# Kernel tuning notes

Measured on AMD Instinct MI355X. Metric: run time of the kernel, lower is better.

## Reference

```python
import jax, jax.numpy as jnp
import numpy as np

# ---- constants mirroring the torch module ----
OSAMP = 8            # temporal oversampling factor
MAX_ITER = 10        # forward solver iterations (LBFGS replaced by fixed GD)
NEG_SHIFT = 2 * OSAMP
OTP = 5              # baseline frames subtracted from ctc/aif
C_SHARP = 500.0      # sharpness constant C=500 in fermi_ir_func
LR = 0.1             # fixed step size for the deterministic forward solve


def interp_linear_1d(x, size):
    # interp_linear_1D: linear upsampling along last (time) axis
    return jax.image.resize(x, x.shape[:-1] + (size,), method='linear')


def fermi_ir(eta, t_os):
    # eta: [B,3,H,W] = (amplitude A, decay rate k, delay t0); t_os: [Tos]
    tsh = t_os - t_os[NEG_SHIFT]                    # negative time shift
    A = eta[:, 0][..., None]                        # [B,H,W,1]
    k = eta[:, 1][..., None]
    t0 = eta[:, 2][..., None]
    step = jax.nn.sigmoid(C_SHARP * tsh)            # sharp causal onset (C=500)
    return A * jax.nn.sigmoid(k * (t0 - tsh)) * step  # [B,H,W,Tos]


def convolve(aif, ir):
    # linear convolution along time via FFT; output aligned with neg_shift offset
    Tos = ir.shape[-1]
    n = 2 * Tos
    Fa = jnp.fft.rfft(aif, n=n, axis=-1)            # [B,1,1,n/2+1]
    Fi = jnp.fft.rfft(ir, n=n, axis=-1)             # [B,H,W,n/2+1]
    full = jnp.fft.irfft(Fa * Fi, n=n, axis=-1)
    return jax.lax.dynamic_slice_in_dim(full, NEG_SHIFT, Tos, axis=-1)


def make_objective(ctc, aif, time, eta_prior, lambda_reg):
    # preprocessing from FermiDataConsLBFGS.forward
    aif = aif - aif[..., :OTP].mean(-1, keepdims=True)
    ctc = ctc - ctc[..., :OTP].mean(-1, keepdims=True)
    Tos = OSAMP * ctc.shape[-1]
    aif_os = interp_linear_1d(aif, Tos)
    ctc_os = interp_linear_1d(ctc, Tos)
    t_os = interp_linear_1d(time, Tos)
    ctc_dc = ctc_os[..., ::OSAMP]                   # [B,H,W,T]
    C_nn = (eta_prior ** 2).sum(axis=(0, 2, 3), keepdims=True)  # [1,3,1,1]
    C_dc = (ctc_dc ** 2).sum()
    sp_lam = jax.nn.softplus(lambda_reg).squeeze()

    def F_obj(eta):  # FermiDConsObj.__call__ (OD disabled: indx_dc = all frames)
        ir = fermi_ir(eta, t_os)
        ctc_est = convolve(aif_os, ir)[..., ::OSAMP] / OSAMP
        dc = ((ctc_dc - ctc_est) ** 2 / C_dc).sum()
        reg = sp_lam * (((eta - eta_prior) ** 2) / C_nn).sum()
        pos = (jax.nn.relu(-eta) ** 2).sum()
        return dc + reg + pos
    return F_obj


def setup_inputs():
    key = jax.random.key(0)
    k1, k2, k3, k4 = jax.random.split(key, 4)
    B, H, W, T = 1, 128, 128, 64
    ctc = jax.random.normal(k1, (B, H, W, T), jnp.float32) * 0.1
    aif = jax.random.uniform(k2, (B, 1, 1, T), jnp.float32)
    time = jnp.arange(T, dtype=jnp.float32)
    seg = jnp.ones((B, H, W), jnp.int32)
    eta_nn = jax.random.uniform(k3, (B, 3, H, W), jnp.float32)
    lambda_reg = jax.random.normal(k4, (1,), jnp.float32)
    return {"ctc": ctc, "aif": aif, "time": time, "seg": seg,
            "eta_nn": eta_nn, "lambda_reg": lambda_reg}


def reference(ctc, aif, time, seg, eta_nn, lambda_reg):
    # seg only affects the (disabled) outlier-detection path
    F_obj = make_objective(ctc, aif, time, eta_nn, lambda_reg)
    gradF = jax.grad(F_obj)

    def step(eta, _):
        return eta - LR * gradF(eta), None

    eta_pi, _ = jax.lax.scan(step, eta_nn, None, length=MAX_ITER)
    return eta_pi
```

## Files before the change

### kernel.cpp

```cpp
#include <hip/hip_runtime.h>
#include <math.h>

#define T_IN 64
#define NPIX 16384
#define MAX_ITER 10
#define NSLOT 43
#define MAGIC 0x13579BDFu

typedef _Float16 half8_t __attribute__((ext_vector_type(8)));
typedef __fp16   fp16x2  __attribute__((ext_vector_type(2)));
typedef float    f32x4   __attribute__((ext_vector_type(4)));
typedef int      i32x4   __attribute__((ext_vector_type(4)));

union H8 { half8_t v; fp16x2 h2[4]; i32x4 i4; };

__device__ __forceinline__ float rcp_fast(float x) { return __builtin_amdgcn_rcpf(x); }

__constant__ constexpr int NTMIN[16] = {0,0,0,0,0,1,1,1,1,2,2,2,2,3,3,3};
__constant__ constexpr int TOFS[16]  = {0,4,8,12,16,20,23,26,29,32,34,36,38,40,41,42};

template<int KT>
__device__ __forceinline__ void buildTile(float T0, float nK, float r, int q,
        const float (&d10b)[16], const float (&tse0)[8], const float (&tse15)[8],
        H8& F0h, H8& F1h, H8& F2h) {
    float  x[8];
    fp16x2 d1h[4];
    float  d10 = T0 - d10b[KT];
    const fp16x2 c1 = {(__fp16)0.25f, (__fp16)0.25f};
    const fp16x2 c2 = {(__fp16)0.50f, (__fp16)0.50f};
    const fp16x2 c3 = {(__fp16)0.75f, (__fp16)0.75f};
    bool arith = true;
    if constexpr (KT == 0 || KT == 15) {
        bool flat = (KT == 0) ? (q == 0) : (q == 3);
        if (flat) {
            arith = false;
            const float* te;
            if constexpr (KT == 0) te = tse0; else te = tse15;
            #pragma unroll
            for (int j = 0; j < 8; ++j) x[j] = __expf(nK * (T0 - te[j]));
            #pragma unroll
            for (int jj = 0; jj < 4; ++jj)
                d1h[jj] = __builtin_amdgcn_cvt_pkrtz(T0 - te[2*jj],
                                                     T0 - te[2*jj+1]);
        }
    }
    if (arith) {
        x[0] = __expf(nK * d10);
        x[4] = __expf(nK * (d10 - 0.5f));
        x[1] = x[0]*r; x[2] = x[1]*r; x[3] = x[2]*r;
        x[5] = x[4]*r; x[6] = x[5]*r; x[7] = x[6]*r;
        fp16x2 D0 = __builtin_amdgcn_cvt_pkrtz(d10, d10 - 0.125f);
        d1h[0] = D0;
        d1h[1] = D0 - c1;
        d1h[2] = D0 - c2;
        d1h[3] = D0 - c3;
    }
    #pragma unroll
    for (int jj = 0; jj < 4; ++jj) {
        float s1a = rcp_fast(1.0f + x[2*jj]);
        float s1b = rcp_fast(1.0f + x[2*jj+1]);
        fp16x2 sh = __builtin_amdgcn_cvt_pkrtz(s1a, s1b);
        fp16x2 eh = sh - sh*sh;
        F0h.h2[jj] = sh;
        F1h.h2[jj] = eh * d1h[jj];
        F2h.h2[jj] = eh;
    }
}

template<int KT>
struct Pipe2 {
    static __device__ __forceinline__ void run(float T0, float nK, float r, int q, int lane,
            const float (&d10b)[16], const float (&tse0)[8], const float (&tse15)[8],
            const i32x4* __restrict__ Bs,
            H8 (&F0p)[2], H8 (&F1p)[2], H8 (&F2p)[2],
            f32x4 (&acc)[3][4]) {
        constexpr int PB = (KT >> 1) & 1;
        if constexpr (KT + 2 < 16)
            buildTile<KT+2>(T0, nK, r, q, d10b, tse0, tse15,
                            F0p[PB^1], F1p[PB^1], F2p[PB^1]);
        const f32x4 Z = (f32x4){0.f, 0.f, 0.f, 0.f};
        #pragma unroll
        for (int nt = NTMIN[KT]; nt < 4; ++nt) {
            int slot = TOFS[KT] + nt - NTMIN[KT];
            H8 bh; bh.i4 = Bs[slot*64 + lane];
            if constexpr (KT < 2) {
                acc[0][nt] = __builtin_amdgcn_mfma_f32_16x16x32_f16(F0p[PB].v, bh.v, Z, 0, 0, 0);
                acc[1][nt] = __builtin_amdgcn_mfma_f32_16x16x32_f16(F1p[PB].v, bh.v, Z, 0, 0, 0);
                acc[2][nt] = __builtin_amdgcn_mfma_f32_16x16x32_f16(F2p[PB].v, bh.v, Z, 0, 0, 0);
            } else {
                acc[0][nt] = __builtin_amdgcn_mfma_f32_16x16x32_f16(F0p[PB].v, bh.v, acc[0][nt], 0, 0, 0);
                acc[1][nt] = __builtin_amdgcn_mfma_f32_16x16x32_f16(F1p[PB].v, bh.v, acc[1][nt], 0, 0, 0);
                acc[2][nt] = __builtin_amdgcn_mfma_f32_16x16x32_f16(F2p[PB].v, bh.v, acc[2][nt], 0, 0, 0);
            }
        }
        if constexpr (KT + 2 < 16)
            Pipe2<KT+2>::run(T0, nK, r, q, lane, d10b, tse0, tse15, Bs, F0p, F1p, F2p, acc);
    }
};

template<int H>
__device__ __forceinline__ void pipeAcc(float T0, float nK, float r, int q, int lane,
        const float (&d10b)[16], const float (&tse0)[8], const float (&tse15)[8],
        const i32x4* __restrict__ Bs, f32x4 (&acc)[3][4]) {
    H8 F0p[2], F1p[2], F2p[2];
    buildTile<H>(T0, nK, r, q, d10b, tse0, tse15, F0p[0], F1p[0], F2p[0]);
    Pipe2<H>::run(T0, nK, r, q, lane, d10b, tse0, tse15, Bs, F0p, F1p, F2p, acc);
}

template<int H>
__device__ __forceinline__ void sendHalf(const f32x4 (&acc)[3][4],
        float2* __restrict__ xch, int pair, int lane) {
    constexpr int SB = 2 - 2*H;
    float2* xw = xch + ((pair*2 + H)*12)*64 + lane;
    #pragma unroll
    for (int i = 0; i < 3; ++i)
        #pragma unroll
        for (int nt = 0; nt < 4; ++nt)
            xw[(i*4+nt)*64] = make_float2(acc[i][nt][SB], acc[i][nt][SB+1]);
}

template<int H>
__device__ __forceinline__ void finishDots(f32x4 (&acc)[3][4],
        const float2* __restrict__ xch, float (&Gtab)[4][16][4],
        int pair, int lane, int q, int n,
        const float (&dcreg)[4][4], float A) {
    constexpr int KB = 2*H;
    const float2* xr = xch + ((pair*2 + (1-H))*12)*64 + lane;
    #pragma unroll
    for (int i = 0; i < 3; ++i)
        #pragma unroll
        for (int nt = 0; nt < 4; ++nt) {
            float2 v = xr[(i*4+nt)*64];
            acc[i][nt][KB]   += v.x;
            acc[i][nt][KB+1] += v.y;
        }
    float Ap0 = __shfl(A, q*4 + KB);
    float Ap1 = __shfl(A, q*4 + KB + 1);
    float SA0=0.f,SK0=0.f,ST0=0.f, SA1=0.f,SK1=0.f,ST1=0.f;
    #pragma unroll
    for (int nt = 0; nt < 4; ++nt) {
        float Y0 = acc[0][nt][KB], Y1 = acc[1][nt][KB], Y2 = acc[2][nt][KB];
        float rr = fmaf(Ap0, Y0, -dcreg[nt][KB]);
        SA0 = fmaf(rr, Y0, SA0); SK0 = fmaf(rr, Y1, SK0); ST0 = fmaf(rr, Y2, ST0);
        float y0 = acc[0][nt][KB+1], y1 = acc[1][nt][KB+1], y2 = acc[2][nt][KB+1];
        float r2 = fmaf(Ap1, y0, -dcreg[nt][KB+1]);
        SA1 = fmaf(r2, y0, SA1); SK1 = fmaf(r2, y1, SK1); ST1 = fmaf(r2, y2, ST1);
    }
    #pragma unroll
    for (int m = 1; m < 16; m <<= 1) {
        SA0 += __shfl_xor(SA0, m); SK0 += __shfl_xor(SK0, m); ST0 += __shfl_xor(ST0, m);
        SA1 += __shfl_xor(SA1, m); SK1 += __shfl_xor(SK1, m); ST1 += __shfl_xor(ST1, m);
    }
    if (n == 0) {
        float* g = Gtab[pair][q*4 + KB];
        g[0] = SA0; g[1] = SK0; g[2] = ST0;
    }
    if (n == 1) {
        float* g = Gtab[pair][q*4 + KB + 1];
        g[0] = SA1; g[1] = SK1; g[2] = ST1;
    }
}

__global__ __launch_bounds__(512, 2) void k_all(
        const float* __restrict__ ctc,  const float* __restrict__ aif,
        const float* __restrict__ timev,const float* __restrict__ lam,
        const float* __restrict__ eta,  unsigned int* __restrict__ flags,
        f32x4* __restrict__ partials,   float* __restrict__ out) {
    __shared__ i32x4 Bs[NSLOT * 64];
    __shared__ float tshs[512];
    __shared__ float aifos[512];
    __shared__ float a_s[64], t_s[64];
    __shared__ f32x4 red[8];
    __shared__ float2 xch[2*4*12*64];
    __shared__ float Gtab[4][16][4];

    const int tid  = threadIdx.x;
    const int lane = tid & 63;
    const int wid  = tid >> 6;
    const int hh   = wid & 1;
    const int pair = wid >> 1;
    const int q = lane >> 4, n = lane & 15;
    const int pixbase = blockIdx.x * 64 + pair * 16;
    const int mypix   = pixbase + n;

    if (tid < 64) { a_s[tid] = aif[tid]; t_s[tid] = timev[tid]; }
    float A  = eta[mypix];
    float K  = eta[NPIX + mypix];
    float T0 = eta[2*NPIX + mypix];
    const float pA = A, pK = K, pT = T0;
    __syncthreads();
    {
        float m5a = 0.2f * (a_s[0]+a_s[1]+a_s[2]+a_s[3]+a_s[4]);
        float t16;
        {
            float xx = 1.5625f; int i0 = (int)xx; float f = xx - (float)i0;
            t16 = t_s[i0]*(1.0f-f) + t_s[i0+1]*f;
        }
        int i = tid;
        float x = ((float)i - 3.5f) * 0.125f;
        float ao, to;
        if (x <= 0.0f)       { ao = a_s[0]  - m5a; to = t_s[0];  }
        else if (x >= 63.0f) { ao = a_s[63] - m5a; to = t_s[63]; }
        else {
            int i0 = (int)x; float f = x - (float)i0;
            ao = (a_s[i0]-m5a)*(1.0f-f) + (a_s[i0+1]-m5a)*f;
            to = t_s[i0]*(1.0f-f) + t_s[i0+1]*f;
        }
        aifos[i] = ao;
        tshs[i]  = to - t16;
    }

    float dcreg[4][4];
    #pragma unroll
    for (int reg = 0; reg < 4; ++reg) {
        const float* cp = ctc + (pixbase + q*4 + reg) * T_IN;
        float m5 = 0.2f * (cp[0]+cp[1]+cp[2]+cp[3]+cp[4]);
        #pragma unroll
        for (int nt = 0; nt < 4; ++nt) {
            int d = nt*16 + n;
            float cc = cp[d] - m5;
            float cm = cp[(d > 0) ? d-1 : 0] - m5;
            dcreg[nt][reg] = (d == 0) ? cc : (0.4375f*cm + 0.5625f*cc);
        }
    }

    {
        float vs = 0.f;
        #pragma unroll
        for (int nt = 0; nt < 4; ++nt)
            #pragma unroll
            for (int r2 = 0; r2 < 4; ++r2) vs += dcreg[nt][r2]*dcreg[nt][r2];
        f32x4 pv = (f32x4){hh ? 0.f : vs, 0.125f*A*A, 0.125f*K*K, 0.125f*T0*T0};
        #pragma unroll
        for (int m = 1; m < 64; m <<= 1) {
            pv.x += __shfl_xor(pv.x, m); pv.y += __shfl_xor(pv.y, m);
            pv.z += __shfl_xor(pv.z, m); pv.w += __shfl_xor(pv.w, m);
        }
        if (lane == 0) red[wid] = pv;
    }
    __syncthreads();
    if (tid == 0) {
        f32x4 s = red[0] + red[1] + red[2] + red[3]
                + red[4] + red[5] + red[6] + red[7];
        partials[blockIdx.x] = s;
        __threadfence();
        __hip_atomic_store(&flags[blockIdx.x], MAGIC, __ATOMIC_RELEASE,
                           __HIP_MEMORY_SCOPE_AGENT);
    }

    for (int idx = tid; idx < NSLOT * 64; idx += 512) {
        int slot = idx >> 6, l = idx & 63;
        int kt, nt;
        if (slot < 20)      { kt = slot >> 2; nt = slot & 3; }
        else if (slot < 32) { int s = slot - 20; int d3 = s / 3; kt = 5 + d3; nt = 1 + (s - 3*d3); }
        else if (slot < 40) { int s = slot - 32; kt = 9 + (s >> 1); nt = 2 + (s & 1); }
        else                { kt = 13 + (slot - 40); nt = 3; }
        int kbase = 32*kt + 8*(l >> 4);
        int m = 16 + 8 * (16*nt + (l & 15));
        H8 bh;
        #pragma unroll
        for (int jj = 0; jj < 4; ++jj) {
            float v[2];
            #pragma unroll
            for (int h = 0; h < 2; ++h) {
                int k  = kbase + 2*jj + h;
                int ai = m - k;
                float s2 = 1.0f / (1.0f + __expf(-500.0f * tshs[k]));
                v[h] = (ai >= 0 && ai < 512) ? s2 * aifos[ai] * 0.125f : 0.0f;
            }
            bh.h2[jj] = (fp16x2){(__fp16)v[0], (__fp16)v[1]};
        }
        Bs[idx] = bh.i4;
    }
    __syncthreads();

    float  d10b[16];
    float  tse0[8], tse15[8];
    #pragma unroll
    for (int kt = 0; kt < 16; ++kt) d10b[kt] = tshs[32*kt + 8*q];
    #pragma unroll
    for (int j = 0; j < 8; ++j) { tse0[j] = tshs[8*q + j]; tse15[j] = tshs[480 + 8*q + j]; }

    if (tid < 256) {
        while (__hip_atomic_load(&flags[tid], __ATOMIC_ACQUIRE,
                                 __HIP_MEMORY_SCOPE_AGENT) != MAGIC)
            __builtin_amdgcn_s_sleep(2);
    }
    __syncthreads();

    f32x4 tot = partials[lane] + partials[64+lane] + partials[128+lane]
              + partials[192+lane];
    #pragma unroll
    for (int m = 1; m < 64; m <<= 1) {
        tot.x += __shfl_xor(tot.x, m); tot.y += __shfl_xor(tot.y, m);
        tot.z += __shfl_xor(tot.z, m); tot.w += __shfl_xor(tot.w, m);
    }
    float spl;
    {
        float xl = lam[0];
        spl = (xl > 0.0f) ? (xl + log1pf(__expf(-xl))) : log1pf(__expf(xl));
    }
    const float cdc2 = 2.0f / tot.x;
    const float rgA  = 2.0f * spl / tot.y;
    const float rgK  = 2.0f * spl / tot.z;
    const float rgT  = 2.0f * spl / tot.w;

    #pragma unroll 1
    for (int it = 0; it < MAX_ITER; ++it) {
        float nK = -K;
        float r  = __expf(0.125f * K);

        f32x4 acc[3][4];
        if (hh == 0) {
            pipeAcc<0>(T0, nK, r, q, lane, d10b, tse0, tse15, Bs, acc);
            sendHalf<0>(acc, xch, pair, lane);
        } else {
            pipeAcc<1>(T0, nK, r, q, lane, d10b, tse0, tse15, Bs, acc);
            sendHalf<1>(acc, xch, pair, lane);
        }
        __syncthreads();
        if (hh == 0) finishDots<0>(acc, xch, Gtab, pair, lane, q, n, dcreg, A);
        else         finishDots<1>(acc, xch, Gtab, pair, lane, q, n, dcreg, A);
        __syncthreads();

        const float GA = Gtab[pair][n][0];
        const float GK = Gtab[pair][n][1];
        const float GT = Gtab[pair][n][2];
        float gA = fmaf(rgA, A  - pA, cdc2 * GA)         + 2.0f * fminf(A,  0.f);
        float gK = fmaf(rgK, K  - pK, cdc2 * A * GK)     + 2.0f * fminf(K,  0.f);
        float gT = fmaf(rgT, T0 - pT, cdc2 * A * K * GT) + 2.0f * fminf(T0, 0.f);
        A  -= 0.1f * gA;
        K  -= 0.1f * gK;
        T0 -= 0.1f * gT;
    }

    if (hh == 0 && lane < 16) {
        out[mypix]          = A;
        out[NPIX + mypix]   = K;
        out[2*NPIX + mypix] = T0;
    }
}

extern "C" void kernel_launch(void* const* d_in, const int* in_sizes, int n_in,
                              void* d_out, int out_size, void* d_ws, size_t ws_size,
                              hipStream_t stream) {
    const float* ctc   = (const float*)d_in[0];
    const float* aif   = (const float*)d_in[1];
    const float* timev = (const float*)d_in[2];
    const float* eta   = (const float*)d_in[4];
    const float* lam   = (const float*)d_in[5];
    float* out = (float*)d_out;
    f32x4*        partials = (f32x4*)d_ws;
    unsigned int* flags    = (unsigned int*)((char*)d_ws + 4096);

    k_all<<<NPIX / 64, 512, 0, stream>>>(ctc, aif, timev, lam, eta,
                                         flags, partials, out);
}
```

Baseline: 117.1 us.

## Split fused kernel into prep and iterate kernels, drop inter-block flag barrier

The single persistent kernel, which used a spin-wait flag barrier across all 256 blocks to get global reductions, is split into two launches. A prep kernel computes the normalisation partials, the shifted time table and the fp16 convolution matrix once (the matrix is spread over 43 blocks instead of being rebuilt in every block) and writes them to workspace. The iterate kernel loads these into LDS and runs the solver. This removes the spin barrier and the redundant per-block matrix build, at the cost of an extra launch and a round trip through global memory.

Result: faster. 106.5 us (-9.1%).

```diff
diff --git a/kernel.cpp b/kernel.cpp
--- a/kernel.cpp
+++ b/kernel.cpp
@@ -5,7 +5,6 @@
 #define NPIX 16384
 #define MAX_ITER 10
 #define NSLOT 43
-#define MAGIC 0x13579BDFu
 
 typedef _Float16 half8_t __attribute__((ext_vector_type(8)));
 typedef __fp16   fp16x2  __attribute__((ext_vector_type(2)));
@@ -161,33 +160,27 @@
     }
 }
 
-__global__ __launch_bounds__(512, 2) void k_all(
+__global__ __launch_bounds__(256, 1) void k_prep(
         const float* __restrict__ ctc,  const float* __restrict__ aif,
-        const float* __restrict__ timev,const float* __restrict__ lam,
-        const float* __restrict__ eta,  unsigned int* __restrict__ flags,
-        f32x4* __restrict__ partials,   float* __restrict__ out) {
-    __shared__ i32x4 Bs[NSLOT * 64];
+        const float* __restrict__ timev,const float* __restrict__ eta,
+        float* __restrict__ tshg, i32x4* __restrict__ Bg,
+        f32x4* __restrict__ partials) {
     __shared__ float tshs[512];
     __shared__ float aifos[512];
     __shared__ float a_s[64], t_s[64];
-    __shared__ f32x4 red[8];
-    __shared__ float2 xch[2*4*12*64];
-    __shared__ float Gtab[4][16][4];
+    __shared__ f32x4 red[4];
 
     const int tid  = threadIdx.x;
     const int lane = tid & 63;
     const int wid  = tid >> 6;
-    const int hh   = wid & 1;
-    const int pair = wid >> 1;
     const int q = lane >> 4, n = lane & 15;
-    const int pixbase = blockIdx.x * 64 + pair * 16;
+    const int pixbase = blockIdx.x * 64 + wid * 16;
     const int mypix   = pixbase + n;
 
     if (tid < 64) { a_s[tid] = aif[tid]; t_s[tid] = timev[tid]; }
     float A  = eta[mypix];
     float K  = eta[NPIX + mypix];
     float T0 = eta[2*NPIX + mypix];
-    const float pA = A, pK = K, pT = T0;
     __syncthreads();
     {
         float m5a = 0.2f * (a_s[0]+a_s[1]+a_s[2]+a_s[3]+a_s[4]);
@@ -196,60 +189,27 @@
             float xx = 1.5625f; int i0 = (int)xx; float f = xx - (float)i0;
             t16 = t_s[i0]*(1.0f-f) + t_s[i0+1]*f;
         }
-        int i = tid;
-        float x = ((float)i - 3.5f) * 0.125f;
-        float ao, to;
-        if (x <= 0.0f)       { ao = a_s[0]  - m5a; to = t_s[0];  }
-        else if (x >= 63.0f) { ao = a_s[63] - m5a; to = t_s[63]; }
-        else {
-            int i0 = (int)x; float f = x - (float)i0;
-            ao = (a_s[i0]-m5a)*(1.0f-f) + (a_s[i0+1]-m5a)*f;
-            to = t_s[i0]*(1.0f-f) + t_s[i0+1]*f;
-        }
-        aifos[i] = ao;
-        tshs[i]  = to - t16;
-    }
-
-    float dcreg[4][4];
-    #pragma unroll
-    for (int reg = 0; reg < 4; ++reg) {
-        const float* cp = ctc + (pixbase + q*4 + reg) * T_IN;
-        float m5 = 0.2f * (cp[0]+cp[1]+cp[2]+cp[3]+cp[4]);
-        #pragma unroll
-        for (int nt = 0; nt < 4; ++nt) {
-            int d = nt*16 + n;
-            float cc = cp[d] - m5;
-            float cm = cp[(d > 0) ? d-1 : 0] - m5;
-            dcreg[nt][reg] = (d == 0) ? cc : (0.4375f*cm + 0.5625f*cc);
-        }
-    }
-
-    {
-        float vs = 0.f;
-        #pragma unroll
-        for (int nt = 0; nt < 4; ++nt)
-            #pragma unroll
-            for (int r2 = 0; r2 < 4; ++r2) vs += dcreg[nt][r2]*dcreg[nt][r2];
-        f32x4 pv = (f32x4){hh ? 0.f : vs, 0.125f*A*A, 0.125f*K*K, 0.125f*T0*T0};
-        #pragma unroll
-        for (int m = 1; m < 64; m <<= 1) {
-            pv.x += __shfl_xor(pv.x, m); pv.y += __shfl_xor(pv.y, m);
-            pv.z += __shfl_xor(pv.z, m); pv.w += __shfl_xor(pv.w, m);
-        }
-        if (lane == 0) red[wid] = pv;
+        #pragma unroll
+        for (int rep = 0; rep < 2; ++rep) {
+            int i = tid + 256*rep;
+            float x = ((float)i - 3.5f) * 0.125f;
+            float ao, to;
+            if (x <= 0.0f)       { ao = a_s[0]  - m5a; to = t_s[0];  }
+            else if (x >= 63.0f) { ao = a_s[63] - m5a; to = t_s[63]; }
+            else {
+                int i0 = (int)x; float f = x - (float)i0;
+                ao = (a_s[i0]-m5a)*(1.0f-f) + (a_s[i0+1]-m5a)*f;
+                to = t_s[i0]*(1.0f-f) + t_s[i0+1]*f;
+            }
+            aifos[i] = ao;
+            tshs[i]  = to - t16;
+            if (blockIdx.x == 0) tshg[i] = to - t16;
+        }
     }
     __syncthreads();
-    if (tid == 0) {
-        f32x4 s = red[0] + red[1] + red[2] + red[3]
-                + red[4] + red[5] + red[6] + red[7];
-        partials[blockIdx.x] = s;
-        __threadfence();
-        __hip_atomic_store(&flags[blockIdx.x], MAGIC, __ATOMIC_RELEASE,
-                           __HIP_MEMORY_SCOPE_AGENT);
-    }
-
-    for (int idx = tid; idx < NSLOT * 64; idx += 512) {
-        int slot = idx >> 6, l = idx & 63;
+
+    if (blockIdx.x < NSLOT && tid < 64) {
+        int slot = blockIdx.x, l = tid;
         int kt, nt;
         if (slot < 20)      { kt = slot >> 2; nt = slot & 3; }
         else if (slot < 32) { int s = slot - 20; int d3 = s / 3; kt = 5 + d3; nt = 1 + (s - 3*d3); }
@@ -270,23 +230,77 @@
             }
             bh.h2[jj] = (fp16x2){(__fp16)v[0], (__fp16)v[1]};
         }
-        Bs[idx] = bh.i4;
+        Bg[slot*64 + l] = bh.i4;
+    }
+
+    float vs = 0.f;
+    #pragma unroll
+    for (int reg = 0; reg < 4; ++reg) {
+        const float* cp = ctc + (pixbase + q*4 + reg) * T_IN;
+        float m5 = 0.2f * (cp[0]+cp[1]+cp[2]+cp[3]+cp[4]);
+        #pragma unroll
+        for (int nt = 0; nt < 4; ++nt) {
+            int d = nt*16 + n;
+            float cc = cp[d] - m5;
+            float cm = cp[(d > 0) ? d-1 : 0] - m5;
+            float dc = (d == 0) ? cc : (0.4375f*cm + 0.5625f*cc);
+            vs += dc * dc;
+        }
+    }
+    {
+        f32x4 pv = (f32x4){vs, 0.25f*A*A, 0.25f*K*K, 0.25f*T0*T0};
+        #pragma unroll
+        for (int m = 1; m < 64; m <<= 1) {
+            pv.x += __shfl_xor(pv.x, m); pv.y += __shfl_xor(pv.y, m);
+            pv.z += __shfl_xor(pv.z, m); pv.w += __shfl_xor(pv.w, m);
+        }
+        if (lane == 0) red[wid] = pv;
     }
     __syncthreads();
-
-    float  d10b[16];
-    float  tse0[8], tse15[8];
-    #pragma unroll
-    for (int kt = 0; kt < 16; ++kt) d10b[kt] = tshs[32*kt + 8*q];
-    #pragma unroll
-    for (int j = 0; j < 8; ++j) { tse0[j] = tshs[8*q + j]; tse15[j] = tshs[480 + 8*q + j]; }
-
-    if (tid < 256) {
-        while (__hip_atomic_load(&flags[tid], __ATOMIC_ACQUIRE,
-                                 __HIP_MEMORY_SCOPE_AGENT) != MAGIC)
-            __builtin_amdgcn_s_sleep(2);
-    }
-    __syncthreads();
+    if (tid == 0)
+        partials[blockIdx.x] = red[0] + red[1] + red[2] + red[3];
+}
+
+__global__ __launch_bounds__(512, 2) void k_iter(
+        const float* __restrict__ ctc,  const float* __restrict__ lam,
+        const float* __restrict__ eta,  const float* __restrict__ tshg,
+        const i32x4* __restrict__ Bg,   const f32x4* __restrict__ partials,
+        float* __restrict__ out) {
+    __shared__ i32x4 Bs[NSLOT * 64];
+    __shared__ float tshs[512];
+    __shared__ float2 xch[2*4*12*64];
+    __shared__ float Gtab[4][16][4];
+
+    const int tid  = threadIdx.x;
+    const int lane = tid & 63;
+    const int wid  = tid >> 6;
+    const int hh   = wid & 1;
+    const int pair = wid >> 1;
+    const int q = lane >> 4, n = lane & 15;
+    const int pixbase = blockIdx.x * 64 + pair * 16;
+    const int mypix   = pixbase + n;
+
+    for (int idx = tid; idx < NSLOT * 64; idx += 512) Bs[idx] = Bg[idx];
+    tshs[tid] = tshg[tid];
+
+    float A  = eta[mypix];
+    float K  = eta[NPIX + mypix];
+    float T0 = eta[2*NPIX + mypix];
+    const float pA = A, pK = K, pT = T0;
+
+    float dcreg[4][4];
+    #pragma unroll
+    for (int reg = 0; reg < 4; ++reg) {
+        const float* cp = ctc + (pixbase + q*4 + reg) * T_IN;
+        float m5 = 0.2f * (cp[0]+cp[1]+cp[2]+cp[3]+cp[4]);
+        #pragma unroll
+        for (int nt = 0; nt < 4; ++nt) {
+            int d = nt*16 + n;
+            float cc = cp[d] - m5;
+            float cm = cp[(d > 0) ? d-1 : 0] - m5;
+            dcreg[nt][reg] = (d == 0) ? cc : (0.4375f*cm + 0.5625f*cc);
+        }
+    }
 
     f32x4 tot = partials[lane] + partials[64+lane] + partials[128+lane]
               + partials[192+lane];
@@ -304,6 +318,15 @@
     const float rgA  = 2.0f * spl / tot.y;
     const float rgK  = 2.0f * spl / tot.z;
     const float rgT  = 2.0f * spl / tot.w;
+
+    __syncthreads();
+
+    float  d10b[16];
+    float  tse0[8], tse15[8];
+    #pragma unroll
+    for (int kt = 0; kt < 16; ++kt) d10b[kt] = tshs[32*kt + 8*q];
+    #pragma unroll
+    for (int j = 0; j < 8; ++j) { tse0[j] = tshs[8*q + j]; tse15[j] = tshs[480 + 8*q + j]; }
 
     #pragma unroll 1
     for (int it = 0; it < MAX_ITER; ++it) {
@@ -350,9 +373,12 @@
     const float* eta   = (const float*)d_in[4];
     const float* lam   = (const float*)d_in[5];
     float* out = (float*)d_out;
-    f32x4*        partials = (f32x4*)d_ws;
-    unsigned int* flags    = (unsigned int*)((char*)d_ws + 4096);
-
-    k_all<<<NPIX / 64, 512, 0, stream>>>(ctc, aif, timev, lam, eta,
-                                         flags, partials, out);
-}
+    f32x4* partials = (f32x4*)d_ws;
+    float* tshg     = (float*)((char*)d_ws + 4096);
+    i32x4* Bg       = (i32x4*)((char*)d_ws + 8192);
+
+    k_prep<<<NPIX / 64, 256, 0, stream>>>(ctc, aif, timev, eta,
+                                          tshg, Bg, partials);
+    k_iter<<<NPIX / 64, 512, 0, stream>>>(ctc, lam, eta, tshg, Bg,
+                                          partials, out);
+}
```
